# Kernel optimization log

Measured on AMD Instinct MI355X. Metric: run time of the kernel, lower is better.

The kernel has to match this reference:

```python
import jax, jax.numpy as jnp
import numpy as np

THRESHOLD = 0.4
MARGIN = 1.0
EPS = 1e-8  # torch F.cosine_similarity norm clamp


def setup_inputs() -> dict:
    key = jax.random.key(0)
    ks = jax.random.split(key, 8)
    B, N, D, T = 4096, 200000, 256, 10
    h_graph = jax.random.normal(ks[0], (B, D), jnp.float32)
    h_sub = jax.random.normal(ks[1], (N, D), jnp.float32)
    sub2graph = jax.random.randint(ks[2], (N,), 0, B, dtype=jnp.int32)
    W1 = jax.random.normal(ks[3], (D, 2 * D), jnp.float32) / np.float32(np.sqrt(D))
    b1 = jnp.zeros((2 * D,), jnp.float32)
    W2 = jax.random.normal(ks[4], (2 * D, 1), jnp.float32) / np.float32(np.sqrt(2 * D))
    b2 = jnp.zeros((1,), jnp.float32)
    Wc = jax.random.normal(ks[5], (2 * D, T), jnp.float32) / np.float32(np.sqrt(2 * D))
    bc = jnp.zeros((T,), jnp.float32)
    return dict(h_graph=h_graph, h_sub=h_sub, W1=W1, b1=b1, W2=W2, b2=b2,
                Wc=Wc, bc=bc, sub2graph=sub2graph)


def _forward(h_graph, h_sub, W1, b1, W2, b2, Wc, bc, sub2graph):
    B = h_graph.shape[0]
    dt = h_sub.dtype
    # SubMaskGenerator: Linear -> ReLU -> (Dropout off, eval) -> Linear -> sigmoid
    subgraph_mask = jax.nn.sigmoid((jax.nn.relu(h_sub @ W1 + b1) @ W2 + b2)[:, 0])  # [N]
    valid = (subgraph_mask > THRESHOLD).astype(dt)               # mask > threshold
    envm = (subgraph_mask <= THRESHOLD - 0.1).astype(dt)         # mask <= threshold-0.1
    # threshold-masked per-graph mean scatter (aggr='mean')
    sum_v = jax.ops.segment_sum(h_sub * valid[:, None], sub2graph, num_segments=B)
    cnt_v = jax.ops.segment_sum(valid, sub2graph, num_segments=B)
    h_sub_aligned = sum_v / jnp.maximum(cnt_v, 1.0)[:, None]     # zeros when no valid subs
    sum_e = jax.ops.segment_sum(h_sub * envm[:, None], sub2graph, num_segments=B)
    cnt_e = jax.ops.segment_sum(envm, sub2graph, num_segments=B)
    h_sub_env = sum_e / jnp.maximum(cnt_e, 1.0)[:, None]
    # pairwise cosine distances (norms clamped like torch)
    an = jnp.maximum(jnp.linalg.norm(h_sub_aligned, axis=-1), EPS)  # [B]
    en = jnp.maximum(jnp.linalg.norm(h_sub_env, axis=-1), EPS)      # [B]
    pos_d = 1.0 - (h_sub_aligned @ h_sub_aligned.T) / (an[:, None] * an[None, :])  # [B,B]
    neg_d = 1.0 - (h_sub_aligned @ h_sub_env.T) / (an[:, None] * en[None, :])      # [B,B]
    nz_pos = jnp.any(h_sub_aligned != 0, axis=1)
    nz_neg = jnp.any(h_sub_env != 0, axis=1)
    pos_num = jnp.maximum(nz_pos.sum() - 1, 1).astype(dt)
    num_env = nz_neg.sum()
    negative = (neg_d * nz_neg[None, :].astype(dt)).sum(1) / jnp.maximum(num_env, 1).astype(dt)
    positive = pos_d.sum(1) / pos_num
    contrib = jax.nn.relu(positive - negative + MARGIN) * nz_pos.astype(dt) * (num_env > 0).astype(dt)
    contrastive_loss = contrib.sum() / B
    out = jnp.concatenate([h_graph, h_sub_aligned], axis=1) @ Wc + bc
    return out, contrastive_loss, subgraph_mask


def reference(h_graph, h_sub, W1, b1, W2, b2, Wc, bc, sub2graph):
    return _forward(h_graph, h_sub, W1, b1, W2, b2, Wc, bc, sub2graph)
```

## Files before the change

### kernel.cpp

```cpp
#include <hip/hip_runtime.h>

#define N_SUB 200000
#define N_GR  4096
#define DIM   256
#define HID   512
#define TCLS  10
#define MROWS 64
#define RCAP  16384
#define RMARG 1e-3f
#define NREP  32

typedef __attribute__((ext_vector_type(8))) short short8;
typedef __attribute__((ext_vector_type(4))) float f32x4;

__device__ __forceinline__ short bf16_rne(float x){
  unsigned u = __builtin_bit_cast(unsigned, x);
  unsigned r = (u + 0x7FFFu + ((u >> 16) & 1u)) >> 16;
  return (short)r;
}
__device__ __forceinline__ float bf16_to_f(short h){
  unsigned u = ((unsigned)(unsigned short)h) << 16;
  return __builtin_bit_cast(float, u);
}
__device__ __forceinline__ float wave_reduce(float v){
  #pragma unroll
  for (int d = 1; d < 64; d <<= 1) v += __shfl_xor(v, d, 64);
  return v;
}
__device__ __forceinline__ int a_gran(int mt, int mrow, int ks, int kgrp){
  return (((((mt*8 + ks)*4 + kgrp)*2 + (mrow>>3)) << 3)
          | ((mrow & 7) ^ ((ks & 3) << 1) ^ (kgrp & 1)));
}

__global__ __launch_bounds__(256) void bconv_kernel(const float* __restrict__ W1,
                                                    short* __restrict__ bth,
                                                    short* __restrict__ btl,
                                                    int* cnt_all, float* S32, float* Se32,
                                                    int* counters, float* loss_p, int* rcnt){
  const int i = blockIdx.x*256 + threadIdx.x;
  if (i < N_GR) cnt_all[i] = 0;
  if (i < NREP*DIM){ S32[i] = 0.f; Se32[i] = 0.f; }
  if (i < 64) loss_p[i] = 0.f;
  if (i < 2) counters[i] = 0;
  if (i == 0) rcnt[0] = 0;
  const int k = i >> 9;
  const int j = i & 511;
  const float x = W1[i];
  const short h = bf16_rne(x);
  const short l = bf16_rne(x - bf16_to_f(h));
  const int nt = j >> 4, mrow = j & 15;
  const int ksg = k >> 5, kgrp = (k >> 3) & 3, kk = k & 7;
  const int lane = kgrp*16 + mrow;
  const size_t dst = (((size_t)(nt*8 + ksg)*64 + lane) << 3) + kk;
  bth[dst] = h;
  btl[dst] = l;
}

__global__ __launch_bounds__(512, 4) void mask_gemm(
    const float* __restrict__ hsub, const short* __restrict__ bth,
    const short* __restrict__ btl, const float* __restrict__ b1,
    const float* __restrict__ W2, const float* __restrict__ b2,
    const int* __restrict__ s2g, float* __restrict__ mask_out,
    int* __restrict__ cnt_all, int* __restrict__ rlist, int* __restrict__ rcnt)
{
  __shared__ short a_hi[16384];
  __shared__ short a_lo[16384];
  __shared__ float sred[512];
  const int tid = threadIdx.x;
  const int lane = tid & 63;
  const int q = tid >> 6;
  const int mrow = lane & 15;
  const int kgrp = lane >> 4;
  const int brow = blockIdx.x*MROWS;

  f32x4 acc[4][4];
  #pragma unroll
  for (int mt=0; mt<4; ++mt)
    #pragma unroll
    for (int nt=0; nt<4; ++nt) acc[mt][nt] = (f32x4){0.f,0.f,0.f,0.f};

  const float* __restrict__ gbase = hsub + (size_t)brow*DIM;
  #pragma unroll
  for (int b = 0; b < 2; ++b){
    float4 g[4];
    #pragma unroll
    for (int i = 0; i < 4; ++i){
      const int idx = (b*4 + i)*512 + tid;
      g[i] = *reinterpret_cast<const float4*>(gbase + (size_t)idx*4);
    }
    #pragma unroll
    for (int i = 0; i < 4; ++i){
      const int idx = (b*4 + i)*512 + tid;
      const int rr = idx >> 6;
      const int ch = idx & 63;
      const float4 v = g[i];
      const short h0=bf16_rne(v.x), h1=bf16_rne(v.y), h2=bf16_rne(v.z), h3=bf16_rne(v.w);
      const short l0=bf16_rne(v.x-bf16_to_f(h0)), l1=bf16_rne(v.y-bf16_to_f(h1));
      const short l2=bf16_rne(v.z-bf16_to_f(h2)), l3=bf16_rne(v.w-bf16_to_f(h3));
      const int so = a_gran(rr>>4, rr&15, ch>>3, (ch>>1)&3)*8 + (ch&1)*4;
      *reinterpret_cast<short4*>(&a_hi[so]) = make_short4(h0,h1,h2,h3);
      *reinterpret_cast<short4*>(&a_lo[so]) = make_short4(l0,l1,l2,l3);
    }
  }
  __syncthreads();

  short8 Ah[4], Al[4];
  #pragma unroll
  for (int ks = 0; ks < 8; ++ks){
    #pragma unroll
    for (int m = 0; m < 4; ++m){
      const int so = a_gran(m, mrow, ks, kgrp)*8;
      Ah[m] = *reinterpret_cast<const short8*>(&a_hi[so]);
      Al[m] = *reinterpret_cast<const short8*>(&a_lo[so]);
    }
    #pragma unroll
    for (int nt = 0; nt < 4; ++nt){
      const size_t bo = (((size_t)((q*4+nt)*8 + ks)*64 + lane) << 3);
      const short8 Bh = *reinterpret_cast<const short8*>(bth + bo);
      const short8 Bl = *reinterpret_cast<const short8*>(btl + bo);
      #pragma unroll
      for (int m = 0; m < 4; ++m){
        acc[m][nt] = __builtin_amdgcn_mfma_f32_16x16x32_bf16(Ah[m], Bh, acc[m][nt], 0,0,0);
        acc[m][nt] = __builtin_amdgcn_mfma_f32_16x16x32_bf16(Ah[m], Bl, acc[m][nt], 0,0,0);
        acc[m][nt] = __builtin_amdgcn_mfma_f32_16x16x32_bf16(Al[m], Bh, acc[m][nt], 0,0,0);
      }
    }
  }

  float w2v[4], b1v[4];
  #pragma unroll
  for (int nt=0; nt<4; ++nt){
    const int n = q*64 + nt*16 + mrow;
    w2v[nt] = W2[n]; b1v[nt] = b1[n];
  }
  #pragma unroll
  for (int mt=0; mt<4; ++mt){
    #pragma unroll
    for (int r=0; r<4; ++r){
      float s = 0.f;
      #pragma unroll
      for (int nt=0; nt<4; ++nt)
        s += fmaxf(acc[mt][nt][r] + b1v[nt], 0.f) * w2v[nt];
      s += __shfl_xor(s, 1, 64);
      s += __shfl_xor(s, 2, 64);
      s += __shfl_xor(s, 4, 64);
      s += __shfl_xor(s, 8, 64);
      if (mrow == 0)
        sred[q*64 + mt*16 + kgrp*4 + r] = s;
    }
  }
  __syncthreads();
  if (tid < MROWS){
    const int rr = brow + tid;
    float tot = b2[0];
    #pragma unroll
    for (int w = 0; w < 8; ++w) tot += sred[w*64 + tid];
    const float m = 1.f / (1.f + expf(-tot));
    mask_out[rr] = m;
    atomicAdd(&cnt_all[s2g[rr]], 1);
    if (fabsf(m - 0.4f) < RMARG || fabsf(m - 0.3f) < RMARG){
      const int p = atomicAdd(rcnt, 1);
      if (p < RCAP) rlist[p] = rr;
    }
  }
}

__global__ __launch_bounds__(512) void refine_kernel(
    const float* __restrict__ hsub, const float* __restrict__ W1,
    const float* __restrict__ b1, const float* __restrict__ W2,
    const float* __restrict__ b2, const int* __restrict__ rlist,
    const int* __restrict__ rcnt, float* __restrict__ mask_out)
{
  __shared__ float arow[256];
  __shared__ float red[512];
  const int n = min(rcnt[0], RCAP);
  const int t = threadIdx.x;
  for (int it = blockIdx.x; it < n; it += gridDim.x){
    const int row = rlist[it];
    if (t < 256) arow[t] = hsub[(size_t)row*DIM + t];
    __syncthreads();
    float y0 = b1[t], y1 = 0.f, y2 = 0.f, y3 = 0.f;
    #pragma unroll 8
    for (int k = 0; k < 64; ++k){
      y0 = fmaf(arow[k],     W1[(size_t)k*512 + t],         y0);
      y1 = fmaf(arow[k+64],  W1[(size_t)(k+64)*512 + t],    y1);
      y2 = fmaf(arow[k+128], W1[(size_t)(k+128)*512 + t],   y2);
      y3 = fmaf(arow[k+192], W1[(size_t)(k+192)*512 + t],   y3);
    }
    const float y = (y0 + y1) + (y2 + y3);
    red[t] = fmaxf(y, 0.f) * W2[t];
    __syncthreads();
    #pragma unroll
    for (int off = 256; off > 0; off >>= 1){
      if (t < off) red[t] += red[t+off];
      __syncthreads();
    }
    if (t == 0) mask_out[row] = 1.f / (1.f + expf(-(red[0] + b2[0])));
    __syncthreads();
  }
}

__global__ __launch_bounds__(1024) void scan_kernel(const int* __restrict__ cnt,
                                                    int* __restrict__ offs,
                                                    int* __restrict__ cursor){
  __shared__ int buf[1024];
  const int t = threadIdx.x;
  const int c0 = cnt[t*4], c1 = cnt[t*4+1], c2 = cnt[t*4+2], c3 = cnt[t*4+3];
  const int s = c0+c1+c2+c3;
  buf[t] = s; __syncthreads();
  for (int d = 1; d < 1024; d <<= 1){
    int v = (t >= d) ? buf[t-d] : 0;
    __syncthreads();
    buf[t] += v;
    __syncthreads();
  }
  const int excl = buf[t] - s;
  const int o0 = excl, o1 = excl+c0, o2 = o1+c1, o3 = o2+c2;
  offs[t*4]=o0; offs[t*4+1]=o1; offs[t*4+2]=o2; offs[t*4+3]=o3;
  cursor[t*4]=o0; cursor[t*4+1]=o1; cursor[t*4+2]=o2; cursor[t*4+3]=o3;
  if (t == 1023) offs[4096] = buf[1023];
}

__global__ void fill_kernel(const int* __restrict__ s2g, int* __restrict__ cursor,
                            int* __restrict__ list){
  const int i = blockIdx.x*blockDim.x + threadIdx.x;
  if (i < N_SUB){
    const int g = s2g[i];
    const int p = atomicAdd(&cursor[g], 1);
    list[p] = i;
  }
}

__global__ __launch_bounds__(256) void graph_means(
    const float* __restrict__ hsub, const float* __restrict__ mask,
    const int* __restrict__ list, const int* __restrict__ offs,
    const float* __restrict__ hgraph, const float* __restrict__ Wc,
    const float* __restrict__ bc, unsigned short* __restrict__ hatAb,
    float* __restrict__ S32, float* __restrict__ Se32,
    int* __restrict__ nzflags, int* __restrict__ counters,
    float* __restrict__ out)
{
  __shared__ int   sidx[256];
  __shared__ unsigned char sflag[256];
  __shared__ float wr4[4][4];
  __shared__ float wrc[TCLS][4];
  const int g = blockIdx.x;
  const int t = threadIdx.x;
  const int w = t >> 6, lane = t & 63;
  const int start = offs[g], end = offs[g+1];
  const int cnt = end - start;
  float sv = 0.f, sev = 0.f;
  int cv = 0, ce = 0;
  for (int base = 0; base < cnt; base += 256){
    const int nb = min(256, cnt - base);
    __syncthreads();
    if (t < nb){
      const int i = list[start + base + t];
      sidx[t] = i;
      const float m = mask[i];
      sflag[t] = (m > 0.4f) ? 1 : ((m <= 0.3f) ? 2 : 0);
    }
    __syncthreads();
    for (int p = 0; p < nb; p += 4){
      const int lim = nb - p;
      const int i0 = sidx[p];
      const int i1 = (lim > 1) ? sidx[p+1] : i0;
      const int i2 = (lim > 2) ? sidx[p+2] : i0;
      const int i3 = (lim > 3) ? sidx[p+3] : i0;
      const int f0 = sflag[p];
      const int f1 = (lim > 1) ? sflag[p+1] : 0;
      const int f2 = (lim > 2) ? sflag[p+2] : 0;
      const int f3 = (lim > 3) ? sflag[p+3] : 0;
      const float v0 = hsub[(size_t)i0*DIM + t];
      const float v1 = hsub[(size_t)i1*DIM + t];
      const float v2 = hsub[(size_t)i2*DIM + t];
      const float v3 = hsub[(size_t)i3*DIM + t];
      if (f0==1){ sv+=v0; cv++; } else if (f0==2){ sev+=v0; ce++; }
      if (f1==1){ sv+=v1; cv++; } else if (f1==2){ sev+=v1; ce++; }
      if (f2==1){ sv+=v2; cv++; } else if (f2==2){ sev+=v2; ce++; }
      if (f3==1){ sv+=v3; cv++; } else if (f3==2){ sev+=v3; ce++; }
    }
  }
  __syncthreads();
  const float aligned = sv  / fmaxf((float)cv, 1.f);
  const float envv    = sev / fmaxf((float)ce, 1.f);
  float r0 = wave_reduce(aligned*aligned);
  float r1 = wave_reduce(envv*envv);
  float r2 = wave_reduce(aligned != 0.f ? 1.f : 0.f);
  float r3 = wave_reduce(envv    != 0.f ? 1.f : 0.f);
  if (lane == 0){ wr4[w][0]=r0; wr4[w][1]=r1; wr4[w][2]=r2; wr4[w][3]=r3; }
  __syncthreads();
  const float an2  = wr4[0][0]+wr4[1][0]+wr4[2][0]+wr4[3][0];
  const float en2  = wr4[0][1]+wr4[1][1]+wr4[2][1]+wr4[3][1];
  const float nzpf = wr4[0][2]+wr4[1][2]+wr4[2][2]+wr4[3][2];
  const float nzef = wr4[0][3]+wr4[1][3]+wr4[2][3]+wr4[3][3];
  const bool nzp = nzpf > 0.f, nze = nzef > 0.f;
  const float an = fmaxf(sqrtf(an2), 1e-8f);
  const float en = fmaxf(sqrtf(en2), 1e-8f);
  const float ha = aligned / an;
  hatAb[(size_t)g*DIM + t] = (unsigned short)bf16_rne(ha);
  atomicAdd(&S32[((g & (NREP-1)) << 8) + t], ha);
  if (nze) atomicAdd(&Se32[((g & (NREP-1)) << 8) + t], envv / en);
  if (t == 0){
    nzflags[g] = nzp ? 1 : 0;
    if (nzp) atomicAdd(&counters[0], 1);
    if (nze) atomicAdd(&counters[1], 1);
  }
  const float hg = hgraph[(size_t)g*DIM + t];
  #pragma unroll
  for (int c = 0; c < TCLS; ++c){
    float part = hg*Wc[t*TCLS+c] + aligned*Wc[(DIM+t)*TCLS+c];
    part = wave_reduce(part);
    if (lane == 0) wrc[c][w] = part;
  }
  __syncthreads();
  if (t < TCLS)
    out[g*TCLS + t] = wrc[t][0]+wrc[t][1]+wrc[t][2]+wrc[t][3] + bc[t];
}

__global__ __launch_bounds__(256) void combine_kernel(const float* __restrict__ S32,
                                                      const float* __restrict__ Se32,
                                                      float* __restrict__ S,
                                                      float* __restrict__ Se){
  const int t = threadIdx.x;
  float s = 0.f, se = 0.f;
  #pragma unroll
  for (int r = 0; r < NREP; ++r){
    s  += S32[r*DIM + t];
    se += Se32[r*DIM + t];
  }
  S[t] = s; Se[t] = se;
}

__global__ __launch_bounds__(256) void loss_kernel(
    const unsigned short* __restrict__ hatAb, const float* __restrict__ S,
    const float* __restrict__ Se, const int* __restrict__ nzflags,
    const int* __restrict__ counters, float* __restrict__ loss_p)
{
  __shared__ float wr[4][2];
  const int g = blockIdx.x, t = threadIdx.x;
  const int w = t >> 6, lane = t & 63;
  const float ha = bf16_to_f((short)hatAb[(size_t)g*DIM + t]);
  float p0 = wave_reduce(ha*S[t]);
  float p1 = wave_reduce(ha*Se[t]);
  if (lane == 0){ wr[w][0] = p0; wr[w][1] = p1; }
  __syncthreads();
  if (t == 0){
    const float dS  = wr[0][0]+wr[1][0]+wr[2][0]+wr[3][0];
    const float dSe = wr[0][1]+wr[1][1]+wr[2][1]+wr[3][1];
    const int nzp_cnt = counters[0];
    const int nenv = counters[1];
    const float pos_num = fmaxf((float)(nzp_cnt - 1), 1.f);
    const float positive = (4096.f - dS) / pos_num;
    const float negative = ((float)nenv - dSe) / fmaxf((float)nenv, 1.f);
    float contrib = fmaxf(positive - negative + 1.f, 0.f);
    contrib *= (nzflags[g] ? 1.f : 0.f) * ((nenv > 0) ? 1.f : 0.f);
    atomicAdd(&loss_p[g & 63], contrib * (1.f/4096.f));
  }
}

__global__ void final_loss(const float* __restrict__ loss_p, float* __restrict__ loss){
  const int t = threadIdx.x;
  float v = loss_p[t];
  v = wave_reduce(v);
  if (t == 0) loss[0] = v;
}

extern "C" void kernel_launch(void* const* d_in, const int* in_sizes, int n_in,
                              void* d_out, int out_size, void* d_ws, size_t ws_size,
                              hipStream_t stream) {
  const float* h_graph = (const float*)d_in[0];
  const float* h_sub   = (const float*)d_in[1];
  const float* W1      = (const float*)d_in[2];
  const float* b1      = (const float*)d_in[3];
  const float* W2      = (const float*)d_in[4];
  const float* b2      = (const float*)d_in[5];
  const float* Wc      = (const float*)d_in[6];
  const float* bc      = (const float*)d_in[7];
  const int*   s2g     = (const int*)d_in[8];

  float* out  = (float*)d_out;
  float* loss = out + N_GR*TCLS;
  float* mask = loss + 1;

  char* ws = (char*)d_ws;
  short* bth    = (short*)ws;
  short* btl    = bth + HID*DIM;
  unsigned short* hatAb = (unsigned short*)(btl + HID*DIM);
  int* cnt_all  = (int*)(hatAb + (size_t)N_GR*DIM);
  int* offs     = cnt_all + N_GR;
  int* cursor   = offs + N_GR + 1;
  int* list     = cursor + N_GR;
  int* nzflags  = list + N_SUB;
  int* counters = nzflags + N_GR;
  int* rcnt     = counters + 2;
  int* rlist    = rcnt + 1;
  float* S      = (float*)(rlist + RCAP);
  float* Se     = S + DIM;
  float* S32    = Se + DIM;
  float* Se32   = S32 + NREP*DIM;
  float* loss_p = Se32 + NREP*DIM;

  hipLaunchKernelGGL(bconv_kernel, dim3(HID*DIM/256), dim3(256), 0, stream,
                     W1, bth, btl, cnt_all, S32, Se32, counters, loss_p, rcnt);
  hipLaunchKernelGGL(mask_gemm, dim3(N_SUB/MROWS), dim3(512), 0, stream,
                     h_sub, bth, btl, b1, W2, b2, s2g, mask, cnt_all, rlist, rcnt);
  hipLaunchKernelGGL(refine_kernel, dim3(384), dim3(512), 0, stream,
                     h_sub, W1, b1, W2, b2, rlist, rcnt, mask);
  hipLaunchKernelGGL(scan_kernel, dim3(1), dim3(1024), 0, stream,
                     cnt_all, offs, cursor);
  hipLaunchKernelGGL(fill_kernel, dim3((N_SUB+255)/256), dim3(256), 0, stream,
                     s2g, cursor, list);
  hipLaunchKernelGGL(graph_means, dim3(N_GR), dim3(256), 0, stream,
                     h_sub, mask, list, offs, h_graph, Wc, bc,
                     hatAb, S32, Se32, nzflags, counters, out);
  hipLaunchKernelGGL(combine_kernel, dim3(1), dim3(256), 0, stream,
                     S32, Se32, S, Se);
  hipLaunchKernelGGL(loss_kernel, dim3(N_GR), dim3(256), 0, stream,
                     hatAb, S, Se, nzflags, counters, loss_p);
  hipLaunchKernelGGL(final_loss, dim3(1), dim3(64), 0, stream,
                     loss_p, loss);
}
```

Before: 393.9 us.

## Widen mask GEMM to 1024-thread blocks and parallelize S reduction

The mask GEMM block grows from 512 to 1024 threads, so each wave covers 2 N-tiles instead of 4 and the whole 64-row A tile loads in one pass. This halves accumulator registers per wave and changes occupancy. The per-graph sum replication count rises from 32 to 128 to reduce atomic contention in graph_means. The single-block combine becomes 16 blocks that accumulate into zero-initialised S and Se with atomics, which makes the float sums order-dependent.

```diff
diff --git a/kernel.cpp b/kernel.cpp
--- a/kernel.cpp
+++ b/kernel.cpp
@@ -8,7 +8,7 @@
 #define MROWS 64
 #define RCAP  16384
 #define RMARG 1e-3f
-#define NREP  32
+#define NREP  128
 
 typedef __attribute__((ext_vector_type(8))) short short8;
 typedef __attribute__((ext_vector_type(4))) float f32x4;
@@ -36,10 +36,12 @@
                                                     short* __restrict__ bth,
                                                     short* __restrict__ btl,
                                                     int* cnt_all, float* S32, float* Se32,
+                                                    float* S, float* Se,
                                                     int* counters, float* loss_p, int* rcnt){
   const int i = blockIdx.x*256 + threadIdx.x;
   if (i < N_GR) cnt_all[i] = 0;
   if (i < NREP*DIM){ S32[i] = 0.f; Se32[i] = 0.f; }
+  if (i < DIM){ S[i] = 0.f; Se[i] = 0.f; }
   if (i < 64) loss_p[i] = 0.f;
   if (i < 2) counters[i] = 0;
   if (i == 0) rcnt[0] = 0;
@@ -56,7 +58,7 @@
   btl[dst] = l;
 }
 
-__global__ __launch_bounds__(512, 4) void mask_gemm(
+__global__ __launch_bounds__(1024) void mask_gemm(
     const float* __restrict__ hsub, const short* __restrict__ bth,
     const short* __restrict__ btl, const float* __restrict__ b1,
     const float* __restrict__ W2, const float* __restrict__ b2,
@@ -65,32 +67,31 @@
 {
   __shared__ short a_hi[16384];
   __shared__ short a_lo[16384];
-  __shared__ float sred[512];
+  __shared__ float sred[1024];
   const int tid = threadIdx.x;
   const int lane = tid & 63;
-  const int q = tid >> 6;
+  const int c = tid >> 6;
   const int mrow = lane & 15;
   const int kgrp = lane >> 4;
   const int brow = blockIdx.x*MROWS;
 
-  f32x4 acc[4][4];
+  f32x4 acc[4][2];
   #pragma unroll
   for (int mt=0; mt<4; ++mt)
     #pragma unroll
-    for (int nt=0; nt<4; ++nt) acc[mt][nt] = (f32x4){0.f,0.f,0.f,0.f};
+    for (int nt=0; nt<2; ++nt) acc[mt][nt] = (f32x4){0.f,0.f,0.f,0.f};
 
   const float* __restrict__ gbase = hsub + (size_t)brow*DIM;
-  #pragma unroll
-  for (int b = 0; b < 2; ++b){
+  {
     float4 g[4];
     #pragma unroll
     for (int i = 0; i < 4; ++i){
-      const int idx = (b*4 + i)*512 + tid;
+      const int idx = i*1024 + tid;
       g[i] = *reinterpret_cast<const float4*>(gbase + (size_t)idx*4);
     }
     #pragma unroll
     for (int i = 0; i < 4; ++i){
-      const int idx = (b*4 + i)*512 + tid;
+      const int idx = i*1024 + tid;
       const int rr = idx >> 6;
       const int ch = idx & 63;
       const float4 v = g[i];
@@ -114,8 +115,9 @@
       Al[m] = *reinterpret_cast<const short8*>(&a_lo[so]);
     }
     #pragma unroll
-    for (int nt = 0; nt < 4; ++nt){
-      const size_t bo = (((size_t)((q*4+nt)*8 + ks)*64 + lane) << 3);
+    for (int nt = 0; nt < 2; ++nt){
+      const int ntg = c*2 + nt;
+      const size_t bo = (((size_t)(ntg*8 + ks)*64 + lane) << 3);
       const short8 Bh = *reinterpret_cast<const short8*>(bth + bo);
       const short8 Bl = *reinterpret_cast<const short8*>(btl + bo);
       #pragma unroll
@@ -127,10 +129,10 @@
     }
   }
 
-  float w2v[4], b1v[4];
-  #pragma unroll
-  for (int nt=0; nt<4; ++nt){
-    const int n = q*64 + nt*16 + mrow;
+  float w2v[2], b1v[2];
+  #pragma unroll
+  for (int nt=0; nt<2; ++nt){
+    const int n = c*32 + nt*16 + mrow;
     w2v[nt] = W2[n]; b1v[nt] = b1[n];
   }
   #pragma unroll
@@ -139,14 +141,14 @@
     for (int r=0; r<4; ++r){
       float s = 0.f;
       #pragma unroll
-      for (int nt=0; nt<4; ++nt)
+      for (int nt=0; nt<2; ++nt)
         s += fmaxf(acc[mt][nt][r] + b1v[nt], 0.f) * w2v[nt];
       s += __shfl_xor(s, 1, 64);
       s += __shfl_xor(s, 2, 64);
       s += __shfl_xor(s, 4, 64);
       s += __shfl_xor(s, 8, 64);
       if (mrow == 0)
-        sred[q*64 + mt*16 + kgrp*4 + r] = s;
+        sred[c*64 + mt*16 + kgrp*4 + r] = s;
     }
   }
   __syncthreads();
@@ -154,7 +156,7 @@
     const int rr = brow + tid;
     float tot = b2[0];
     #pragma unroll
-    for (int w = 0; w < 8; ++w) tot += sred[w*64 + tid];
+    for (int w = 0; w < 16; ++w) tot += sred[w*64 + tid];
     const float m = 1.f / (1.f + expf(-tot));
     mask_out[rr] = m;
     atomicAdd(&cnt_all[s2g[rr]], 1);
@@ -322,14 +324,16 @@
                                                       const float* __restrict__ Se32,
                                                       float* __restrict__ S,
                                                       float* __restrict__ Se){
+  const int b = blockIdx.x;
   const int t = threadIdx.x;
   float s = 0.f, se = 0.f;
   #pragma unroll
-  for (int r = 0; r < NREP; ++r){
-    s  += S32[r*DIM + t];
-    se += Se32[r*DIM + t];
-  }
-  S[t] = s; Se[t] = se;
+  for (int r = 0; r < 8; ++r){
+    s  += S32[(b*8 + r)*DIM + t];
+    se += Se32[(b*8 + r)*DIM + t];
+  }
+  atomicAdd(&S[t], s);
+  atomicAdd(&Se[t], se);
 }
 
 __global__ __launch_bounds__(256) void loss_kernel(
@@ -402,8 +406,8 @@
   float* loss_p = Se32 + NREP*DIM;
 
   hipLaunchKernelGGL(bconv_kernel, dim3(HID*DIM/256), dim3(256), 0, stream,
-                     W1, bth, btl, cnt_all, S32, Se32, counters, loss_p, rcnt);
-  hipLaunchKernelGGL(mask_gemm, dim3(N_SUB/MROWS), dim3(512), 0, stream,
+                     W1, bth, btl, cnt_all, S32, Se32, S, Se, counters, loss_p, rcnt);
+  hipLaunchKernelGGL(mask_gemm, dim3(N_SUB/MROWS), dim3(1024), 0, stream,
                      h_sub, bth, btl, b1, W2, b2, s2g, mask, cnt_all, rlist, rcnt);
   hipLaunchKernelGGL(refine_kernel, dim3(384), dim3(512), 0, stream,
                      h_sub, W1, b1, W2, b2, rlist, rcnt, mask);
@@ -414,7 +418,7 @@
   hipLaunchKernelGGL(graph_means, dim3(N_GR), dim3(256), 0, stream,
                      h_sub, mask, list, offs, h_graph, Wc, bc,
                      hatAb, S32, Se32, nzflags, counters, out);
-  hipLaunchKernelGGL(combine_kernel, dim3(1), dim3(256), 0, stream,
+  hipLaunchKernelGGL(combine_kernel, dim3(16), dim3(256), 0, stream,
                      S32, Se32, S, Se);
   hipLaunchKernelGGL(loss_kernel, dim3(N_GR), dim3(256), 0, stream,
                      hatAb, S, Se, nzflags, counters, loss_p);
```

Result: no change. 398.2 us (+1.1%).
